# Kernel tuning notes

Measured on AMD Instinct MI355X. Metric: run time of the kernel, lower is better.

The kernel has to match this reference:

```python
import jax, jax.numpy as jnp
import numpy as np

DIM = 384
HEADS = 8


def setup_inputs() -> dict:
    key = jax.random.key(0)
    ks = jax.random.split(key, 8)
    d = DIM
    return {
        "x": jax.random.normal(ks[0], (4, d, 128, 128), jnp.float32),
        "message": jax.random.normal(ks[1], (4, d, 128, 128), jnp.float32),
        "temperature": jnp.ones((HEADS, 1, 1), jnp.float32),
        "qkv_w": jax.random.normal(ks[2], (3 * d, d), jnp.float32) * 0.02,   # 1x1 conv weight
        "dw_w": jax.random.normal(ks[3], (3 * d, 1, 3, 3), jnp.float32) * 0.02,  # depthwise 3x3
        "proj_w": jax.random.normal(ks[4], (d, d), jnp.float32) * 0.02,     # project_out 1x1
        "lin_w": jax.random.normal(ks[5], (d, 2 * d), jnp.float32) * 0.02,  # nn.Linear weight [out,in]
        "lin_b": jnp.zeros((d,), jnp.float32),
    }


def _qkv_branch(t, qkv_w, dw_w):
    # 1x1 conv (pointwise) then depthwise 3x3, groups = 3*dim
    y = jnp.einsum('oc,bchw->bohw', qkv_w, t)
    y = jax.lax.conv_general_dilated(
        y, dw_w, window_strides=(1, 1), padding='SAME',
        dimension_numbers=('NCHW', 'OIHW', 'NCHW'),
        feature_group_count=dw_w.shape[0])
    return jnp.split(y, 3, axis=1)  # q, k, v each [b, dim, h, w]


def _to_heads(t):
    b, c, h, w = t.shape
    return t.reshape(b, HEADS, c // HEADS, h * w)  # [b, head, c, n]


def _l2norm(t):
    # torch F.normalize(dim=-1, eps=1e-12)
    n = jnp.sqrt(jnp.sum(t * t, axis=-1, keepdims=True))
    return t / jnp.maximum(n, 1e-12)


def reference(x, message, temperature, qkv_w, dw_w, proj_w, lin_w, lin_b):
    b, c, h, w = x.shape
    q, k, v = (_to_heads(t) for t in _qkv_branch(x, qkv_w, dw_w))
    q_m, k_m, v_m = (_to_heads(t) for t in _qkv_branch(message, qkv_w, dw_w))

    k_c = jnp.concatenate([k, k_m], axis=2)   # [b, head, 2c, n]
    v_c = jnp.concatenate([v, v_m], axis=2)

    q = _l2norm(q)
    k_c = _l2norm(k_c)
    q_m = _l2norm(q_m)

    # channel attention: [b, head, c, 2c]
    attn1 = jax.nn.softmax(jnp.einsum('bhcn,bhdn->bhcd', q, k_c) * temperature, axis=-1)
    attn2 = jax.nn.softmax(jnp.einsum('bhcn,bhdn->bhcd', q_m, k_c) * temperature, axis=-1)

    out1 = jnp.einsum('bhcd,bhdn->bhcn', attn1, v_c)  # [b, head, c, n]
    out2 = jnp.einsum('bhcd,bhdn->bhcn', attn2, v_c)

    # 'b head c (h w) -> b (h w) (head c)'
    out1 = out1.transpose(0, 3, 1, 2).reshape(b, h * w, c)
    out2 = out2.transpose(0, 3, 1, 2).reshape(b, h * w, c)

    cat = jnp.concatenate([out1, out2], axis=2)  # [b, n, 2c]
    out = cat @ lin_w.T + lin_b                  # [b, n, c]

    # 'b (h w) c -> b c h w'
    out = out.transpose(0, 2, 1).reshape(b, c, h, w)
    out = jnp.einsum('oc,bchw->bohw', proj_w, out)
    return out
```

## Files before the change

kernel.cpp:

```cpp
#include <hip/hip_runtime.h>

typedef unsigned short u16;
typedef unsigned int u32;

#define BATCH 4
#define CDIM 384
#define IMG 128
#define HW 16384
#define QKVC 1152
#define NHEADS 8
#define CHD 48
#define DD2 96
#define KFIN 768

typedef __attribute__((ext_vector_type(8))) short bf16x8;
typedef __attribute__((ext_vector_type(4))) float f32x4;

__device__ __forceinline__ u16 f2bf(float f){
  union { float f; u32 u; } v; v.f = f;
  u32 u = v.u;
  u32 r = (u + 0x7fffu + ((u >> 16) & 1u)) >> 16;
  return (u16)r;
}
__device__ __forceinline__ float bf2f(u16 h){
  union { u32 u; float f; } v; v.u = ((u32)h) << 16;
  return v.f;
}

#define OFF_QKVX  ((size_t)0)
#define OFF_QKVM  ((size_t)150994944)
#define OFF_T     ((size_t)301989888)
#define OFF_SSQ   ((size_t)339738624)
#define OFF_S     ((size_t)339775488)
#define OFF_ATTN  ((size_t)340955136)
#define OFF_AFINB ((size_t)342134784)
#define OFF_W2    ((size_t)344494080)
#define OFF_B2    ((size_t)345673728)
#define OFF_WB    ((size_t)345675264)

typedef __attribute__((address_space(1))) const u32 gas_u32;
typedef __attribute__((address_space(3))) u32 las_u32;
__device__ __forceinline__ void gl_lds16(const u16* g, u16* l){
  __builtin_amdgcn_global_load_lds((gas_u32*)g, (las_u32*)l, 16, 0, 0);
}

__global__ void __launch_bounds__(256) k_w2(const float* __restrict__ proj,
                                            const float* __restrict__ lin,
                                            const float* __restrict__ linb,
                                            const float* __restrict__ qkvw,
                                            float* __restrict__ W2,
                                            float* __restrict__ b2,
                                            u16* __restrict__ Wb){
  int idx = blockIdx.x * 256 + threadIdx.x;
  if (idx < CDIM * KFIN){
    int o = idx / KFIN, d = idx % KFIN;
    float acc = 0.f;
    for (int c = 0; c < CDIM; c++)
      acc = fmaf(proj[o * CDIM + c], lin[c * KFIN + d], acc);
    W2[idx] = acc;
  }
  if (idx < CDIM){
    float acc = 0.f;
    for (int c = 0; c < CDIM; c++)
      acc = fmaf(proj[idx * CDIM + c], linb[c], acc);
    b2[idx] = acc;
  }
  if (idx < QKVC * CDIM) Wb[idx] = f2bf(qkvw[idx]);
}

__global__ void __launch_bounds__(256) k_cvt(const float* __restrict__ x,
                                             const float* __restrict__ msg,
                                             u16* __restrict__ Bt){
  int z = blockIdx.z;
  const float* src = (z < 4 ? x : msg) + (size_t)(z & 3) * CDIM * HW;
  u16* dst = Bt + (size_t)z * HW * CDIM;
  int nb = blockIdx.x * 64, cb = blockIdx.y * 64;
  __shared__ u16 t[64][65];
  int tid = threadIdx.x;
  #pragma unroll
  for (int i = 0; i < 16; i++){
    int idx = tid + i * 256;
    int c = idx >> 6, n = idx & 63;
    t[c][n] = f2bf(src[(size_t)(cb + c) * HW + nb + n]);
  }
  __syncthreads();
  u32* d32 = (u32*)dst;
  #pragma unroll
  for (int i = 0; i < 8; i++){
    int idx = tid + i * 256;
    int n = idx >> 5, cp = idx & 31;
    u32 v = (u32)t[2 * cp][n] | ((u32)t[2 * cp + 1][n] << 16);
    d32[((size_t)(nb + n) * CDIM + cb) / 2 + cp] = v;
  }
}

__global__ void __launch_bounds__(256) k_pw(const u16* __restrict__ A,
                                            const u16* __restrict__ B,
                                            u16* __restrict__ C){
  __shared__ __align__(16) u16 As[2 * 4096];
  __shared__ __align__(16) u16 Bs[2 * 4096];
  int orig = blockIdx.x;
  int swz = (orig & 7) * 144 + (orig >> 3);
  int bx = swz % 9, by = swz / 9;
  int m0 = bx * 128, n0 = by * 128;
  int tid = threadIdx.x;
  int w = tid >> 6, lane = tid & 63;
  int wy = w >> 1, wx = w & 1;
  int lm = lane & 15, q = lane >> 4;

  int srow = w * 16 + (lane >> 2);
  int scol = (lane & 3) * 8;
  const u16* ga = A + (size_t)(m0 + srow) * CDIM + scol;
  const u16* gb = B + (size_t)(n0 + srow) * CDIM + scol;
  u16* la = As + srow * 32 + scol;
  u16* lb = Bs + srow * 32 + scol;

  f32x4 acc[4][4];
  #pragma unroll
  for (int i = 0; i < 4; i++)
    #pragma unroll
    for (int j = 0; j < 4; j++) acc[i][j] = (f32x4){0.f,0.f,0.f,0.f};

#define PW_STAGE(buf, k0) do{ \
    gl_lds16(ga + (k0),             la + (buf) * 4096); \
    gl_lds16(ga + 64*CDIM + (k0),   la + (buf) * 4096 + 2048); \
    gl_lds16(gb + (k0),             lb + (buf) * 4096); \
    gl_lds16(gb + 64*CDIM + (k0),   lb + (buf) * 4096 + 2048); \
  }while(0)

  PW_STAGE(0, 0);
  __syncthreads();
  int cur = 0;
  for (int t = 0; t < 12; t++){
    if (t < 11) PW_STAGE(cur ^ 1, (t + 1) * 32);
    bf16x8 af[4], bfr[4];
    #pragma unroll
    for (int i = 0; i < 4; i++)
      af[i] = *(const bf16x8*)&As[cur * 4096 + (wy * 64 + i * 16 + lm) * 32 + q * 8];
    #pragma unroll
    for (int j = 0; j < 4; j++)
      bfr[j] = *(const bf16x8*)&Bs[cur * 4096 + (wx * 64 + j * 16 + lm) * 32 + q * 8];
    #pragma unroll
    for (int i = 0; i < 4; i++)
      #pragma unroll
      for (int j = 0; j < 4; j++)
        acc[i][j] = __builtin_amdgcn_mfma_f32_16x16x32_bf16(af[i], bfr[j], acc[i][j], 0, 0, 0);
    __syncthreads();
    cur ^= 1;
  }
#undef PW_STAGE
  #pragma unroll
  for (int i = 0; i < 4; i++){
    #pragma unroll
    for (int r = 0; r < 4; r++){
      int row = m0 + wy * 64 + i * 16 + q * 4 + r;
      u16* cp = C + (size_t)row * HW + n0 + wx * 64 + lm;
      #pragma unroll
      for (int j = 0; j < 4; j++)
        cp[j * 16] = f2bf(acc[i][j][r]);
    }
  }
}

__device__ __forceinline__ void loadrow(const u16* __restrict__ src, int r, int cg, float* o){
  if ((unsigned)r >= IMG){
    #pragma unroll
    for (int i = 0; i < 18; i++) o[i] = 0.f;
    return;
  }
  const u16* p = src + (size_t)r * IMG + cg * 16;
  uint4 v0 = *(const uint4*)p;
  uint4 v1 = *(const uint4*)(p + 8);
  u32 ww[8] = {v0.x, v0.y, v0.z, v0.w, v1.x, v1.y, v1.z, v1.w};
  #pragma unroll
  for (int i = 0; i < 8; i++){
    union { u32 u; float f; } lo, hi;
    lo.u = ww[i] << 16;
    hi.u = ww[i] & 0xffff0000u;
    o[1 + 2 * i] = lo.f;
    o[2 + 2 * i] = hi.f;
  }
  o[0]  = (cg > 0) ? bf2f(p[-1]) : 0.f;
  o[17] = (cg < 7) ? bf2f(p[16]) : 0.f;
}

__global__ void __launch_bounds__(256) k_dw2(const u16* __restrict__ T,
                                             const float* __restrict__ dw,
                                             u16* __restrict__ qdst,
                                             u16* __restrict__ vdst,
                                             float* __restrict__ ssq){
  int ch = blockIdx.x;
  const u16* src = T + (size_t)ch * HW;
  u16* dst = (ch < 2 * CDIM) ? qdst + (size_t)ch * HW
                             : vdst + (size_t)(ch - 2 * CDIM) * HW;
  float w[9];
  #pragma unroll
  for (int t = 0; t < 9; t++) w[t] = dw[ch * 9 + t];
  int tid = threadIdx.x;
  int rg = tid >> 3, cg = tid & 7;
  float ss = 0.f;
  #pragma unroll
  for (int rr = 0; rr < 4; rr++){
    int r = rg * 4 + rr;
    float a[18], b[18], c[18];
    loadrow(src, r - 1, cg, a);
    loadrow(src, r,     cg, b);
    loadrow(src, r + 1, cg, c);
    u32 pk[8];
    #pragma unroll
    for (int x = 0; x < 16; x++){
      float acc = w[0] * a[x];
      acc = fmaf(w[1], a[x + 1], acc);
      acc = fmaf(w[2], a[x + 2], acc);
      acc = fmaf(w[3], b[x],     acc);
      acc = fmaf(w[4], b[x + 1], acc);
      acc = fmaf(w[5], b[x + 2], acc);
      acc = fmaf(w[6], c[x],     acc);
      acc = fmaf(w[7], c[x + 1], acc);
      acc = fmaf(w[8], c[x + 2], acc);
      ss = fmaf(acc, acc, ss);
      u16 hv = f2bf(acc);
      if (x & 1) pk[x >> 1] |= (u32)hv << 16;
      else       pk[x >> 1]  = (u32)hv;
    }
    *(uint4*)(dst + (size_t)r * IMG + cg * 16)     = *(uint4*)&pk[0];
    *(uint4*)(dst + (size_t)r * IMG + cg * 16 + 8) = *(uint4*)&pk[4];
  }
  if (ch < 2 * CDIM){
    __shared__ float red[256];
    red[tid] = ss;
    __syncthreads();
    for (int s = 128; s > 0; s >>= 1){
      if (tid < s) red[tid] += red[tid + s];
      __syncthreads();
    }
    if (tid == 0) ssq[ch] = red[0];
  }
}

__global__ void __launch_bounds__(256) k_vt(const u16* __restrict__ Bt,
                                            u16* __restrict__ qkvx,
                                            u16* __restrict__ qkvm){
  int z = blockIdx.z;
  int inp = z >> 2, b = z & 3;
  const u16* vcn = Bt + (size_t)z * HW * CDIM;
  int h = blockIdx.y;
  int n0 = blockIdx.x * 128;
  u16* vt = (h < 4 ? qkvx : qkvm) + ((size_t)b * QKVC + 2 * CDIM) * HW;
  int dbase = (h & 3) * 96 + inp * 48;
  __shared__ u16 tile[48][136];
  int tid = threadIdx.x;
  #pragma unroll
  for (int j = 0; j < 3; j++){
    int i = tid + j * 256;
    int row = i >> 4, c8 = i & 15;
    uint4 v = *(const uint4*)(vcn + (size_t)(h * 48 + row) * HW + n0 + c8 * 8);
    *(uint4*)&tile[row][c8 * 8] = v;
  }
  __syncthreads();
  int n = tid >> 1, half = tid & 1;
  u16* dstp = vt + (size_t)(n0 + n) * CDIM + dbase + half * 24;
  #pragma unroll
  for (int u = 0; u < 3; u++){
    u32 pk[4];
    #pragma unroll
    for (int p = 0; p < 4; p++){
      int c = half * 24 + u * 8 + p * 2;
      pk[p] = (u32)tile[c][n] | ((u32)tile[c + 1][n] << 16);
    }
    *(uint4*)(dstp + u * 8) = *(uint4*)pk;
  }
}

#define LCHUNK 1024
__global__ void __launch_bounds__(256) k_logits_mfma(const u16* __restrict__ qkvx,
                                                     const u16* __restrict__ qkvm,
                                                     float* __restrict__ S){
  int nc = blockIdx.x;
  int bh = blockIdx.y;
  int b = bh & 3, h = bh >> 2;
  int tid = threadIdx.x;
  int w = tid >> 6, lane = tid & 63;
  int wy = w >> 1, wx = w & 1;
  int lm = lane & 15, quad = lane >> 4;

  const u16* ap[3]; const u16* bp[3];
  #pragma unroll
  for (int i = 0; i < 3; i++){
    int g = wy * 48 + i * 16 + lm;
    int c = (g < 48) ? g : g - 48;
    ap[i] = ((g < 48) ? qkvx : qkvm) + ((size_t)b * QKVC + h * CHD + c) * HW;
    int d = wx * 48 + i * 16 + lm;
    int cc = (d < 48) ? d : d - 48;
    bp[i] = ((d < 48) ? qkvx : qkvm) + ((size_t)b * QKVC + CDIM + h * CHD + cc) * HW;
  }
  f32x4 acc[3][3];
  #pragma unroll
  for (int i = 0; i < 3; i++)
    #pragma unroll
    for (int j = 0; j < 3; j++) acc[i][j] = (f32x4){0.f,0.f,0.f,0.f};

  int nbeg = nc * LCHUNK + quad * 8;
  int nend = nc * LCHUNK + LCHUNK;
  for (int n = nbeg; n < nend; n += 32){
    bf16x8 af[3], bfr[3];
    #pragma unroll
    for (int i = 0; i < 3; i++) af[i]  = *(const bf16x8*)(ap[i] + n);
    #pragma unroll
    for (int j = 0; j < 3; j++) bfr[j] = *(const bf16x8*)(bp[j] + n);
    #pragma unroll
    for (int i = 0; i < 3; i++)
      #pragma unroll
      for (int j = 0; j < 3; j++)
        acc[i][j] = __builtin_amdgcn_mfma_f32_16x16x32_bf16(af[i], bfr[j], acc[i][j], 0, 0, 0);
  }
  #pragma unroll
  for (int i = 0; i < 3; i++){
    #pragma unroll
    for (int r = 0; r < 4; r++){
      int g = wy * 48 + i * 16 + quad * 4 + r;
      int iq = (g >= 48) ? 1 : 0;
      int c = iq ? g - 48 : g;
      float* Sp = S + (((size_t)(iq * BATCH + b) * NHEADS + h) * CHD + c) * DD2;
      #pragma unroll
      for (int j = 0; j < 3; j++)
        atomicAdd(&Sp[wx * 48 + j * 16 + lm], acc[i][j][r]);
    }
  }
}

__global__ void __launch_bounds__(128) k_softmax(const float* __restrict__ S,
                                                 const float* __restrict__ ssq,
                                                 const float* __restrict__ temp,
                                                 float* __restrict__ attn){
  int row = blockIdx.x;
  int c = row % CHD;
  int h = (row / CHD) % NHEADS;
  int b = (row / (CHD * NHEADS)) % BATCH;
  int iq = row / (CHD * NHEADS * BATCH);
  int tid = threadIdx.x;
  __shared__ float sh[128];
  const float* Sp = S + (size_t)row * DD2;
  float ssq_q = ssq[(iq * BATCH + b) * QKVC + h * CHD + c];
  float nq = fmaxf(sqrtf(ssq_q), 1e-12f);
  float tmp = temp[h];
  float logit = -1e30f;
  int d = tid;
  if (d < DD2){
    float ssq_k = ssq[((d < CHD ? 0 : 1) * BATCH + b) * QKVC + CDIM + h * CHD + (d % CHD)];
    float nk = fmaxf(sqrtf(ssq_k), 1e-12f);
    logit = Sp[d] * tmp / (nq * nk);
  }
  sh[tid] = logit; __syncthreads();
  for (int s = 64; s > 0; s >>= 1){
    if (tid < s) sh[tid] = fmaxf(sh[tid], sh[tid + s]);
    __syncthreads();
  }
  float mx = sh[0]; __syncthreads();
  float e = (d < DD2) ? expf(logit - mx) : 0.f;
  sh[tid] = e; __syncthreads();
  for (int s = 64; s > 0; s >>= 1){
    if (tid < s) sh[tid] += sh[tid + s];
    __syncthreads();
  }
  float sum = sh[0];
  if (d < DD2) attn[(size_t)row * DD2 + d] = e / sum;
}

__global__ void __launch_bounds__(128) k_mmat(const float* __restrict__ attn,
                                              const float* __restrict__ W2,
                                              u16* __restrict__ AfinB){
  int oz = blockIdx.x;
  int h = blockIdx.y;
  int b = blockIdx.z;
  __shared__ float a1[CHD * DD2];
  __shared__ float a2[CHD * DD2];
  int tid = threadIdx.x;
  const float* A1 = attn + ((size_t)(0 * BATCH + b) * NHEADS + h) * CHD * DD2;
  const float* A2 = attn + ((size_t)(1 * BATCH + b) * NHEADS + h) * CHD * DD2;
  for (int i = tid; i < CHD * DD2; i += 128){ a1[i] = A1[i]; a2[i] = A2[i]; }
  __syncthreads();
  int e = tid;
  if (e < DD2){
    for (int oo = 0; oo < 8; oo++){
      int o = oz * 8 + oo;
      float acc = 0.f;
      #pragma unroll 4
      for (int cc = 0; cc < CHD; cc++){
        acc = fmaf(W2[o * KFIN + h * CHD + cc],        a1[cc * DD2 + e], acc);
        acc = fmaf(W2[o * KFIN + CDIM + h * CHD + cc], a2[cc * DD2 + e], acc);
      }
      AfinB[((size_t)b * CDIM + o) * KFIN + h * DD2 + e] = f2bf(acc);
    }
  }
}

__global__ void __launch_bounds__(256) k_fin(const u16* __restrict__ AfB,
                                             const u16* __restrict__ qkvx,
                                             const u16* __restrict__ qkvm,
                                             const float* __restrict__ b2,
                                             float* __restrict__ out){
  __shared__ __align__(16) u16 As[2 * 4096];
  __shared__ __align__(16) u16 Bs[2 * 4096];
  int orig = blockIdx.x;
  int swz = (orig & 7) * 192 + (orig >> 3);
  int m = swz % 3;
  int rest = swz / 3;
  int n0 = (rest & 127) * 128;
  int bz = rest >> 7;
  int m0 = m * 128;
  int tid = threadIdx.x;
  int w = tid >> 6, lane = tid & 63;
  int wy = w >> 1, wx = w & 1;
  int lm = lane & 15, q = lane >> 4;

  int srow = w * 16 + (lane >> 2);
  int scol = (lane & 3) * 8;
  const u16* A = AfB + (size_t)bz * CDIM * KFIN;
  const u16* ga  = A + (size_t)(m0 + srow) * KFIN + scol;
  const u16* gb0 = qkvx + ((size_t)bz * QKVC + 2 * CDIM) * HW + (size_t)(n0 + srow) * CDIM + scol;
  const u16* gb1 = qkvm + ((size_t)bz * QKVC + 2 * CDIM) * HW + (size_t)(n0 + srow) * CDIM + scol;
  u16* la = As + srow * 32 + scol;
  u16* lb = Bs + srow * 32 + scol;

  f32x4 acc[4][4];
  #pragma unroll
  for (int i = 0; i < 4; i++)
    #pragma unroll
    for (int j = 0; j < 4; j++) acc[i][j] = (f32x4){0.f,0.f,0.f,0.f};

#define FIN_STAGE(buf, t) do{ \
    int hp_ = (t) >= 12; \
    int k0_ = ((t) - hp_ * 12) * 32; \
    const u16* gb_ = hp_ ? gb1 : gb0; \
    gl_lds16(ga + hp_ * CDIM + k0_,            la + (buf) * 4096); \
    gl_lds16(ga + hp_ * CDIM + k0_ + 64*KFIN,  la + (buf) * 4096 + 2048); \
    gl_lds16(gb_ + k0_,                        lb + (buf) * 4096); \
    gl_lds16(gb_ + k0_ + 64*CDIM,              lb + (buf) * 4096 + 2048); \
  }while(0)

  FIN_STAGE(0, 0);
  __syncthreads();
  int cur = 0;
  for (int t = 0; t < 24; t++){
    if (t < 23) FIN_STAGE(cur ^ 1, t + 1);
    bf16x8 af[4], bfr[4];
    #pragma unroll
    for (int i = 0; i < 4; i++)
      af[i] = *(const bf16x8*)&As[cur * 4096 + (wy * 64 + i * 16 + lm) * 32 + q * 8];
    #pragma unroll
    for (int j = 0; j < 4; j++)
      bfr[j] = *(const bf16x8*)&Bs[cur * 4096 + (wx * 64 + j * 16 + lm) * 32 + q * 8];
    #pragma unroll
    for (int i = 0; i < 4; i++)
      #pragma unroll
      for (int j = 0; j < 4; j++)
        acc[i][j] = __builtin_amdgcn_mfma_f32_16x16x32_bf16(af[i], bfr[j], acc[i][j], 0, 0, 0);
    __syncthreads();
    cur ^= 1;
  }
#undef FIN_STAGE
  #pragma unroll
  for (int i = 0; i < 4; i++){
    #pragma unroll
    for (int r = 0; r < 4; r++){
      int row = m0 + wy * 64 + i * 16 + q * 4 + r;
      float bv = b2[row];
      float* cp = out + (size_t)bz * CDIM * HW + (size_t)row * HW + n0 + wx * 64 + lm;
      #pragma unroll
      for (int j = 0; j < 4; j++)
        cp[j * 16] = acc[i][j][r] + bv;
    }
  }
}

extern "C" void kernel_launch(void* const* d_in, const int* in_sizes, int n_in,
                              void* d_out, int out_size, void* d_ws, size_t ws_size,
                              hipStream_t stream){
  const float* x      = (const float*)d_in[0];
  const float* msg    = (const float*)d_in[1];
  const float* temp   = (const float*)d_in[2];
  const float* qkv_w  = (const float*)d_in[3];
  const float* dw_w   = (const float*)d_in[4];
  const float* proj_w = (const float*)d_in[5];
  const float* lin_w  = (const float*)d_in[6];
  const float* lin_b  = (const float*)d_in[7];
  float* out = (float*)d_out;

  char* ws = (char*)d_ws;
  u16*   qkvx  = (u16*)(ws + OFF_QKVX);
  u16*   qkvm  = (u16*)(ws + OFF_QKVM);
  u16*   T     = (u16*)(ws + OFF_T);
  float* ssq   = (float*)(ws + OFF_SSQ);
  float* S     = (float*)(ws + OFF_S);
  float* attn  = (float*)(ws + OFF_ATTN);
  u16*   AfinB = (u16*)(ws + OFF_AFINB);
  float* W2    = (float*)(ws + OFF_W2);
  float* b2    = (float*)(ws + OFF_B2);
  u16*   Wb    = (u16*)(ws + OFF_WB);

  u16* Bt = (u16*)d_out;

  hipMemsetAsync(ws + OFF_S, 0, (OFF_ATTN - OFF_S), stream);

  k_w2<<<dim3((QKVC * CDIM + 255) / 256), dim3(256), 0, stream>>>(
      proj_w, lin_w, lin_b, qkv_w, W2, b2, Wb);

  k_cvt<<<dim3(HW / 64, CDIM / 64, 8), dim3(256), 0, stream>>>(x, msg, Bt);

  for (int z = 0; z < 8; z++){
    int inp = z >> 2, bb = z & 3;
    u16* qdst = (inp ? qkvm : qkvx) + (size_t)bb * QKVC * HW;
    k_pw<<<dim3(QKVC / 128 * (HW / 128)), dim3(256), 0, stream>>>(
        Wb, Bt + (size_t)z * HW * CDIM, T);
    k_dw2<<<dim3(QKVC), dim3(256), 0, stream>>>(
        T, dw_w, qdst, Bt + (size_t)z * HW * CDIM, ssq + (size_t)z * QKVC);
  }

  k_vt<<<dim3(HW / 128, 8, 8), dim3(256), 0, stream>>>(Bt, qkvx, qkvm);

  k_logits_mfma<<<dim3(16, 32), dim3(256), 0, stream>>>(qkvx, qkvm, S);
  k_softmax<<<dim3(2 * BATCH * NHEADS * CHD), dim3(128), 0, stream>>>(S, ssq, temp, attn);
  k_mmat<<<dim3(CDIM / 8, NHEADS, BATCH), dim3(128), 0, stream>>>(attn, W2, AfinB);
  k_fin<<<dim3(3 * (HW / 128) * BATCH), dim3(256), 0, stream>>>(
      AfinB, qkvx, qkvm, b2, out);
}
```

Baseline: 1.017 ms.

## Software-pipeline convert, pointwise GEMM and depthwise conv across fused stage launches

Replaces the per-batch sequence of convert, pointwise GEMM and depthwise kernels with ten launches of one staged kernel. Each launch runs the convert for item t, the GEMM for item t-1 and the depthwise conv for item t-2 concurrently. The GEMM output is double-buffered, with the unused V region of qkvm serving as the second buffer. The V transpose is also fused with the logits kernel into one launch, the depthwise conv reuses rows through a sliding window, and the convert uses float4 loads. The aim is to cut launch count and fill the GPU with independent work, at the cost of more complex block dispatch and higher shared-memory and register pressure in the merged kernel.

```diff
diff --git a/kernel.cpp b/kernel.cpp
--- a/kernel.cpp
+++ b/kernel.cpp
@@ -42,6 +42,13 @@
 typedef __attribute__((address_space(3))) u32 las_u32;
 __device__ __forceinline__ void gl_lds16(const u16* g, u16* l){
   __builtin_amdgcn_global_load_lds((gas_u32*)g, (las_u32*)l, 16, 0, 0);
+}
+
+__device__ __forceinline__ u16* t_row(u16* T0, u16* qkvm, int par, int ch){
+  if (par == 0) return T0 + (size_t)ch * HW;
+  int bq = ch / 384;
+  int rr = ch - bq * 384;
+  return qkvm + ((size_t)bq * QKVC + 2 * CDIM + rr) * HW;
 }
 
 __global__ void __launch_bounds__(256) k_w2(const float* __restrict__ proj,
@@ -68,100 +75,6 @@
   if (idx < QKVC * CDIM) Wb[idx] = f2bf(qkvw[idx]);
 }
 
-__global__ void __launch_bounds__(256) k_cvt(const float* __restrict__ x,
-                                             const float* __restrict__ msg,
-                                             u16* __restrict__ Bt){
-  int z = blockIdx.z;
-  const float* src = (z < 4 ? x : msg) + (size_t)(z & 3) * CDIM * HW;
-  u16* dst = Bt + (size_t)z * HW * CDIM;
-  int nb = blockIdx.x * 64, cb = blockIdx.y * 64;
-  __shared__ u16 t[64][65];
-  int tid = threadIdx.x;
-  #pragma unroll
-  for (int i = 0; i < 16; i++){
-    int idx = tid + i * 256;
-    int c = idx >> 6, n = idx & 63;
-    t[c][n] = f2bf(src[(size_t)(cb + c) * HW + nb + n]);
-  }
-  __syncthreads();
-  u32* d32 = (u32*)dst;
-  #pragma unroll
-  for (int i = 0; i < 8; i++){
-    int idx = tid + i * 256;
-    int n = idx >> 5, cp = idx & 31;
-    u32 v = (u32)t[2 * cp][n] | ((u32)t[2 * cp + 1][n] << 16);
-    d32[((size_t)(nb + n) * CDIM + cb) / 2 + cp] = v;
-  }
-}
-
-__global__ void __launch_bounds__(256) k_pw(const u16* __restrict__ A,
-                                            const u16* __restrict__ B,
-                                            u16* __restrict__ C){
-  __shared__ __align__(16) u16 As[2 * 4096];
-  __shared__ __align__(16) u16 Bs[2 * 4096];
-  int orig = blockIdx.x;
-  int swz = (orig & 7) * 144 + (orig >> 3);
-  int bx = swz % 9, by = swz / 9;
-  int m0 = bx * 128, n0 = by * 128;
-  int tid = threadIdx.x;
-  int w = tid >> 6, lane = tid & 63;
-  int wy = w >> 1, wx = w & 1;
-  int lm = lane & 15, q = lane >> 4;
-
-  int srow = w * 16 + (lane >> 2);
-  int scol = (lane & 3) * 8;
-  const u16* ga = A + (size_t)(m0 + srow) * CDIM + scol;
-  const u16* gb = B + (size_t)(n0 + srow) * CDIM + scol;
-  u16* la = As + srow * 32 + scol;
-  u16* lb = Bs + srow * 32 + scol;
-
-  f32x4 acc[4][4];
-  #pragma unroll
-  for (int i = 0; i < 4; i++)
-    #pragma unroll
-    for (int j = 0; j < 4; j++) acc[i][j] = (f32x4){0.f,0.f,0.f,0.f};
-
-#define PW_STAGE(buf, k0) do{ \
-    gl_lds16(ga + (k0),             la + (buf) * 4096); \
-    gl_lds16(ga + 64*CDIM + (k0),   la + (buf) * 4096 + 2048); \
-    gl_lds16(gb + (k0),             lb + (buf) * 4096); \
-    gl_lds16(gb + 64*CDIM + (k0),   lb + (buf) * 4096 + 2048); \
-  }while(0)
-
-  PW_STAGE(0, 0);
-  __syncthreads();
-  int cur = 0;
-  for (int t = 0; t < 12; t++){
-    if (t < 11) PW_STAGE(cur ^ 1, (t + 1) * 32);
-    bf16x8 af[4], bfr[4];
-    #pragma unroll
-    for (int i = 0; i < 4; i++)
-      af[i] = *(const bf16x8*)&As[cur * 4096 + (wy * 64 + i * 16 + lm) * 32 + q * 8];
-    #pragma unroll
-    for (int j = 0; j < 4; j++)
-      bfr[j] = *(const bf16x8*)&Bs[cur * 4096 + (wx * 64 + j * 16 + lm) * 32 + q * 8];
-    #pragma unroll
-    for (int i = 0; i < 4; i++)
-      #pragma unroll
-      for (int j = 0; j < 4; j++)
-        acc[i][j] = __builtin_amdgcn_mfma_f32_16x16x32_bf16(af[i], bfr[j], acc[i][j], 0, 0, 0);
-    __syncthreads();
-    cur ^= 1;
-  }
-#undef PW_STAGE
-  #pragma unroll
-  for (int i = 0; i < 4; i++){
-    #pragma unroll
-    for (int r = 0; r < 4; r++){
-      int row = m0 + wy * 64 + i * 16 + q * 4 + r;
-      u16* cp = C + (size_t)row * HW + n0 + wx * 64 + lm;
-      #pragma unroll
-      for (int j = 0; j < 4; j++)
-        cp[j * 16] = f2bf(acc[i][j][r]);
-    }
-  }
-}
-
 __device__ __forceinline__ void loadrow(const u16* __restrict__ src, int r, int cg, float* o){
   if ((unsigned)r >= IMG){
     #pragma unroll
@@ -184,147 +97,261 @@
   o[17] = (cg < 7) ? bf2f(p[16]) : 0.f;
 }
 
-__global__ void __launch_bounds__(256) k_dw2(const u16* __restrict__ T,
-                                             const float* __restrict__ dw,
-                                             u16* __restrict__ qdst,
-                                             u16* __restrict__ vdst,
-                                             float* __restrict__ ssq){
-  int ch = blockIdx.x;
-  const u16* src = T + (size_t)ch * HW;
-  u16* dst = (ch < 2 * CDIM) ? qdst + (size_t)ch * HW
-                             : vdst + (size_t)(ch - 2 * CDIM) * HW;
-  float w[9];
-  #pragma unroll
-  for (int t = 0; t < 9; t++) w[t] = dw[ch * 9 + t];
+__global__ void __launch_bounds__(256) k_stage(
+    int t, int npw, int ndw,
+    const u16* __restrict__ Wb, u16* __restrict__ Bt,
+    u16* __restrict__ T0, u16* __restrict__ qkvx, u16* __restrict__ qkvm,
+    const float* __restrict__ x, const float* __restrict__ msg,
+    const float* __restrict__ dww, float* __restrict__ ssq){
+  __shared__ __align__(16) u16 smem[16384];
+  int bid = blockIdx.x;
   int tid = threadIdx.x;
-  int rg = tid >> 3, cg = tid & 7;
-  float ss = 0.f;
-  #pragma unroll
-  for (int rr = 0; rr < 4; rr++){
-    int r = rg * 4 + rr;
-    float a[18], b[18], c[18];
-    loadrow(src, r - 1, cg, a);
-    loadrow(src, r,     cg, b);
-    loadrow(src, r + 1, cg, c);
-    u32 pk[8];
-    #pragma unroll
-    for (int x = 0; x < 16; x++){
-      float acc = w[0] * a[x];
-      acc = fmaf(w[1], a[x + 1], acc);
-      acc = fmaf(w[2], a[x + 2], acc);
-      acc = fmaf(w[3], b[x],     acc);
-      acc = fmaf(w[4], b[x + 1], acc);
-      acc = fmaf(w[5], b[x + 2], acc);
-      acc = fmaf(w[6], c[x],     acc);
-      acc = fmaf(w[7], c[x + 1], acc);
-      acc = fmaf(w[8], c[x + 2], acc);
-      ss = fmaf(acc, acc, ss);
-      u16 hv = f2bf(acc);
-      if (x & 1) pk[x >> 1] |= (u32)hv << 16;
-      else       pk[x >> 1]  = (u32)hv;
-    }
-    *(uint4*)(dst + (size_t)r * IMG + cg * 16)     = *(uint4*)&pk[0];
-    *(uint4*)(dst + (size_t)r * IMG + cg * 16 + 8) = *(uint4*)&pk[4];
-  }
-  if (ch < 2 * CDIM){
-    __shared__ float red[256];
-    red[tid] = ss;
+
+  if (bid < npw){
+    int z = t - 1, par = z & 1;
+    const u16* B = Bt + (size_t)z * HW * CDIM;
+    u16* As = smem;
+    u16* Bs = smem + 8192;
+    int swz = (bid & 7) * 144 + (bid >> 3);
+    int bx = swz % 9, by = swz / 9;
+    int m0 = bx * 128, n0 = by * 128;
+    int w = tid >> 6, lane = tid & 63;
+    int wy = w >> 1, wx = w & 1;
+    int lm = lane & 15, q = lane >> 4;
+
+    int srow = w * 16 + (lane >> 2);
+    int scol = (lane & 3) * 8;
+    const u16* ga = Wb + (size_t)(m0 + srow) * CDIM + scol;
+    const u16* gb = B + (size_t)(n0 + srow) * CDIM + scol;
+    u16* la = As + srow * 32 + scol;
+    u16* lb = Bs + srow * 32 + scol;
+
+    f32x4 acc[4][4];
+    #pragma unroll
+    for (int i = 0; i < 4; i++)
+      #pragma unroll
+      for (int j = 0; j < 4; j++) acc[i][j] = (f32x4){0.f,0.f,0.f,0.f};
+
+#define PW_STAGE(buf, k0) do{ \
+      gl_lds16(ga + (k0),             la + (buf) * 4096); \
+      gl_lds16(ga + 64*CDIM + (k0),   la + (buf) * 4096 + 2048); \
+      gl_lds16(gb + (k0),             lb + (buf) * 4096); \
+      gl_lds16(gb + 64*CDIM + (k0),   lb + (buf) * 4096 + 2048); \
+    }while(0)
+
+    PW_STAGE(0, 0);
     __syncthreads();
-    for (int s = 128; s > 0; s >>= 1){
-      if (tid < s) red[tid] += red[tid + s];
+    int cur = 0;
+    for (int kt = 0; kt < 12; kt++){
+      if (kt < 11) PW_STAGE(cur ^ 1, (kt + 1) * 32);
+      bf16x8 af[4], bfr[4];
+      #pragma unroll
+      for (int i = 0; i < 4; i++)
+        af[i] = *(const bf16x8*)&As[cur * 4096 + (wy * 64 + i * 16 + lm) * 32 + q * 8];
+      #pragma unroll
+      for (int j = 0; j < 4; j++)
+        bfr[j] = *(const bf16x8*)&Bs[cur * 4096 + (wx * 64 + j * 16 + lm) * 32 + q * 8];
+      #pragma unroll
+      for (int i = 0; i < 4; i++)
+        #pragma unroll
+        for (int j = 0; j < 4; j++)
+          acc[i][j] = __builtin_amdgcn_mfma_f32_16x16x32_bf16(af[i], bfr[j], acc[i][j], 0, 0, 0);
       __syncthreads();
-    }
-    if (tid == 0) ssq[ch] = red[0];
-  }
-}
-
-__global__ void __launch_bounds__(256) k_vt(const u16* __restrict__ Bt,
-                                            u16* __restrict__ qkvx,
-                                            u16* __restrict__ qkvm){
-  int z = blockIdx.z;
-  int inp = z >> 2, b = z & 3;
-  const u16* vcn = Bt + (size_t)z * HW * CDIM;
-  int h = blockIdx.y;
-  int n0 = blockIdx.x * 128;
-  u16* vt = (h < 4 ? qkvx : qkvm) + ((size_t)b * QKVC + 2 * CDIM) * HW;
-  int dbase = (h & 3) * 96 + inp * 48;
+      cur ^= 1;
+    }
+#undef PW_STAGE
+    #pragma unroll
+    for (int i = 0; i < 4; i++){
+      #pragma unroll
+      for (int r = 0; r < 4; r++){
+        int row = m0 + wy * 64 + i * 16 + q * 4 + r;
+        u16* cp = t_row(T0, qkvm, par, row) + n0 + wx * 64 + lm;
+        #pragma unroll
+        for (int j = 0; j < 4; j++)
+          cp[j * 16] = f2bf(acc[i][j][r]);
+      }
+    }
+
+  } else if (bid < npw + ndw){
+    int ch = bid - npw;
+    int z = t - 2, par = z & 1;
+    const u16* src = t_row(T0, qkvm, par, ch);
+    u16* dst;
+    if (ch < 2 * CDIM){
+      u16* qd = ((z >> 2) ? qkvm : qkvx) + (size_t)(z & 3) * QKVC * HW;
+      dst = qd + (size_t)ch * HW;
+    } else {
+      dst = Bt + (size_t)z * HW * CDIM + (size_t)(ch - 2 * CDIM) * HW;
+    }
+    float w[9];
+    #pragma unroll
+    for (int t9 = 0; t9 < 9; t9++) w[t9] = dww[ch * 9 + t9];
+    int rg = tid >> 3, cg = tid & 7;
+    int r0 = rg * 4;
+    float ra[18], rb[18], rc[18];
+    loadrow(src, r0 - 1, cg, ra);
+    loadrow(src, r0,     cg, rb);
+    float ss = 0.f;
+    #pragma unroll
+    for (int rr = 0; rr < 4; rr++){
+      int r = r0 + rr;
+      loadrow(src, r + 1, cg, rc);
+      u32 pk[8];
+      #pragma unroll
+      for (int xx = 0; xx < 16; xx++){
+        float a2 = w[0] * ra[xx];
+        a2 = fmaf(w[1], ra[xx + 1], a2);
+        a2 = fmaf(w[2], ra[xx + 2], a2);
+        a2 = fmaf(w[3], rb[xx],     a2);
+        a2 = fmaf(w[4], rb[xx + 1], a2);
+        a2 = fmaf(w[5], rb[xx + 2], a2);
+        a2 = fmaf(w[6], rc[xx],     a2);
+        a2 = fmaf(w[7], rc[xx + 1], a2);
+        a2 = fmaf(w[8], rc[xx + 2], a2);
+        ss = fmaf(a2, a2, ss);
+        u16 hv = f2bf(a2);
+        if (xx & 1) pk[xx >> 1] |= (u32)hv << 16;
+        else        pk[xx >> 1]  = (u32)hv;
+      }
+      *(uint4*)(dst + (size_t)r * IMG + cg * 16)     = *(uint4*)&pk[0];
+      *(uint4*)(dst + (size_t)r * IMG + cg * 16 + 8) = *(uint4*)&pk[4];
+      #pragma unroll
+      for (int ii = 0; ii < 18; ii++){ ra[ii] = rb[ii]; rb[ii] = rc[ii]; }
+    }
+    if (ch < 2 * CDIM){
+      float* red = (float*)smem;
+      red[tid] = ss;
+      __syncthreads();
+      for (int s = 128; s > 0; s >>= 1){
+        if (tid < s) red[tid] += red[tid + s];
+        __syncthreads();
+      }
+      if (tid == 0) ssq[(size_t)z * QKVC + ch] = red[0];
+    }
+
+  } else {
+    int cb = bid - npw - ndw;
+    int z = t;
+    const float* src = (z < 4 ? x : msg) + (size_t)(z & 3) * CDIM * HW;
+    u16* dstz = Bt + (size_t)z * HW * CDIM;
+    int n0 = (cb & 127) * 128;
+    int c0 = (cb >> 7) * 64;
+    u16 (*tile)[130] = (u16(*)[130])smem;
+    #pragma unroll
+    for (int i = 0; i < 8; i++){
+      int c = (tid >> 5) + i * 8;
+      int nq = tid & 31;
+      float4 v = *(const float4*)(src + (size_t)(c0 + c) * HW + n0 + nq * 4);
+      u32 p0 = (u32)f2bf(v.x) | ((u32)f2bf(v.y) << 16);
+      u32 p1 = (u32)f2bf(v.z) | ((u32)f2bf(v.w) << 16);
+      *(u32*)&tile[c][nq * 4]     = p0;
+      *(u32*)&tile[c][nq * 4 + 2] = p1;
+    }
+    __syncthreads();
+    #pragma unroll
+    for (int u = 0; u < 2; u++){
+      int idx = tid + u * 256;
+      int n = idx >> 2, j = idx & 3;
+      u32 pk[8];
+      #pragma unroll
+      for (int p = 0; p < 8; p++)
+        pk[p] = (u32)tile[j * 16 + 2 * p][n] | ((u32)tile[j * 16 + 2 * p + 1][n] << 16);
+      u16* dp = dstz + (size_t)(n0 + n) * CDIM + c0 + j * 16;
+      *(uint4*)dp       = *(uint4*)&pk[0];
+      *(uint4*)(dp + 8) = *(uint4*)&pk[4];
+    }
+  }
+}
+
+#define LCHUNK 1024
+__global__ void __launch_bounds__(256) k_tail(u16* __restrict__ qkvx,
+                                              u16* __restrict__ qkvm,
+                                              float* __restrict__ S,
+                                              const u16* __restrict__ Bt){
   __shared__ u16 tile[48][136];
+  int bid = blockIdx.x;
   int tid = threadIdx.x;
-  #pragma unroll
-  for (int j = 0; j < 3; j++){
-    int i = tid + j * 256;
-    int row = i >> 4, c8 = i & 15;
-    uint4 v = *(const uint4*)(vcn + (size_t)(h * 48 + row) * HW + n0 + c8 * 8);
-    *(uint4*)&tile[row][c8 * 8] = v;
-  }
-  __syncthreads();
-  int n = tid >> 1, half = tid & 1;
-  u16* dstp = vt + (size_t)(n0 + n) * CDIM + dbase + half * 24;
-  #pragma unroll
-  for (int u = 0; u < 3; u++){
-    u32 pk[4];
-    #pragma unroll
-    for (int p = 0; p < 4; p++){
-      int c = half * 24 + u * 8 + p * 2;
-      pk[p] = (u32)tile[c][n] | ((u32)tile[c + 1][n] << 16);
-    }
-    *(uint4*)(dstp + u * 8) = *(uint4*)pk;
-  }
-}
-
-#define LCHUNK 1024
-__global__ void __launch_bounds__(256) k_logits_mfma(const u16* __restrict__ qkvx,
-                                                     const u16* __restrict__ qkvm,
-                                                     float* __restrict__ S){
-  int nc = blockIdx.x;
-  int bh = blockIdx.y;
-  int b = bh & 3, h = bh >> 2;
-  int tid = threadIdx.x;
-  int w = tid >> 6, lane = tid & 63;
-  int wy = w >> 1, wx = w & 1;
-  int lm = lane & 15, quad = lane >> 4;
-
-  const u16* ap[3]; const u16* bp[3];
-  #pragma unroll
-  for (int i = 0; i < 3; i++){
-    int g = wy * 48 + i * 16 + lm;
-    int c = (g < 48) ? g : g - 48;
-    ap[i] = ((g < 48) ? qkvx : qkvm) + ((size_t)b * QKVC + h * CHD + c) * HW;
-    int d = wx * 48 + i * 16 + lm;
-    int cc = (d < 48) ? d : d - 48;
-    bp[i] = ((d < 48) ? qkvx : qkvm) + ((size_t)b * QKVC + CDIM + h * CHD + cc) * HW;
-  }
-  f32x4 acc[3][3];
-  #pragma unroll
-  for (int i = 0; i < 3; i++)
-    #pragma unroll
-    for (int j = 0; j < 3; j++) acc[i][j] = (f32x4){0.f,0.f,0.f,0.f};
-
-  int nbeg = nc * LCHUNK + quad * 8;
-  int nend = nc * LCHUNK + LCHUNK;
-  for (int n = nbeg; n < nend; n += 32){
-    bf16x8 af[3], bfr[3];
-    #pragma unroll
-    for (int i = 0; i < 3; i++) af[i]  = *(const bf16x8*)(ap[i] + n);
-    #pragma unroll
-    for (int j = 0; j < 3; j++) bfr[j] = *(const bf16x8*)(bp[j] + n);
+
+  if (bid < 512){
+    int nc = bid & 15;
+    int bh = bid >> 4;
+    int b = bh & 3, h = bh >> 2;
+    int w = tid >> 6, lane = tid & 63;
+    int wy = w >> 1, wx = w & 1;
+    int lm = lane & 15, quad = lane >> 4;
+
+    const u16* ap[3]; const u16* bp[3];
+    #pragma unroll
+    for (int i = 0; i < 3; i++){
+      int g = wy * 48 + i * 16 + lm;
+      int c = (g < 48) ? g : g - 48;
+      ap[i] = ((g < 48) ? qkvx : qkvm) + ((size_t)b * QKVC + h * CHD + c) * HW;
+      int d = wx * 48 + i * 16 + lm;
+      int cc = (d < 48) ? d : d - 48;
+      bp[i] = ((d < 48) ? qkvx : qkvm) + ((size_t)b * QKVC + CDIM + h * CHD + cc) * HW;
+    }
+    f32x4 acc[3][3];
     #pragma unroll
     for (int i = 0; i < 3; i++)
       #pragma unroll
-      for (int j = 0; j < 3; j++)
-        acc[i][j] = __builtin_amdgcn_mfma_f32_16x16x32_bf16(af[i], bfr[j], acc[i][j], 0, 0, 0);
-  }
-  #pragma unroll
-  for (int i = 0; i < 3; i++){
-    #pragma unroll
-    for (int r = 0; r < 4; r++){
-      int g = wy * 48 + i * 16 + quad * 4 + r;
-      int iq = (g >= 48) ? 1 : 0;
-      int c = iq ? g - 48 : g;
-      float* Sp = S + (((size_t)(iq * BATCH + b) * NHEADS + h) * CHD + c) * DD2;
-      #pragma unroll
-      for (int j = 0; j < 3; j++)
-        atomicAdd(&Sp[wx * 48 + j * 16 + lm], acc[i][j][r]);
+      for (int j = 0; j < 3; j++) acc[i][j] = (f32x4){0.f,0.f,0.f,0.f};
+
+    int nbeg = nc * LCHUNK + quad * 8;
+    int nend = nc * LCHUNK + LCHUNK;
+    for (int n = nbeg; n < nend; n += 32){
+      bf16x8 af[3], bfr[3];
+      #pragma unroll
+      for (int i = 0; i < 3; i++) af[i]  = *(const bf16x8*)(ap[i] + n);
+      #pragma unroll
+      for (int j = 0; j < 3; j++) bfr[j] = *(const bf16x8*)(bp[j] + n);
+      #pragma unroll
+      for (int i = 0; i < 3; i++)
+        #pragma unroll
+        for (int j = 0; j < 3; j++)
+          acc[i][j] = __builtin_amdgcn_mfma_f32_16x16x32_bf16(af[i], bfr[j], acc[i][j], 0, 0, 0);
+    }
+    #pragma unroll
+    for (int i = 0; i < 3; i++){
+      #pragma unroll
+      for (int r = 0; r < 4; r++){
+        int g = wy * 48 + i * 16 + quad * 4 + r;
+        int iq = (g >= 48) ? 1 : 0;
+        int c = iq ? g - 48 : g;
+        float* Sp = S + (((size_t)(iq * BATCH + b) * NHEADS + h) * CHD + c) * DD2;
+        #pragma unroll
+        for (int j = 0; j < 3; j++)
+          atomicAdd(&Sp[wx * 48 + j * 16 + lm], acc[i][j][r]);
+      }
+    }
+  } else {
+    int v = bid - 512;
+    int nb = v & 127;
+    int h = (v >> 7) & 7;
+    int z = v >> 10;
+    int inp = z >> 2, b = z & 3;
+    const u16* vcn = Bt + (size_t)z * HW * CDIM;
+    int n0 = nb * 128;
+    u16* vt = (h < 4 ? qkvx : qkvm) + ((size_t)b * QKVC + 2 * CDIM) * HW;
+    int dbase = (h & 3) * 96 + inp * 48;
+    #pragma unroll
+    for (int j = 0; j < 3; j++){
+      int i = tid + j * 256;
+      int row = i >> 4, c8 = i & 15;
+      uint4 vv = *(const uint4*)(vcn + (size_t)(h * 48 + row) * HW + n0 + c8 * 8);
+      *(uint4*)&tile[row][c8 * 8] = vv;
+    }
+    __syncthreads();
+    int n = tid >> 1, half = tid & 1;
+    u16* dstp = vt + (size_t)(n0 + n) * CDIM + dbase + half * 24;
+    #pragma unroll
+    for (int u = 0; u < 3; u++){
+      u32 pk[4];
+      #pragma unroll
+      for (int p = 0; p < 4; p++){
+        int c = half * 24 + u * 8 + p * 2;
+        pk[p] = (u32)tile[c][n] | ((u32)tile[c + 1][n] << 16);
+      }
+      *(uint4*)(dstp + u * 8) = *(uint4*)pk;
     }
   }
 }
@@ -490,7 +517,7 @@
   char* ws = (char*)d_ws;
   u16*   qkvx  = (u16*)(ws + OFF_QKVX);
   u16*   qkvm  = (u16*)(ws + OFF_QKVM);
-  u16*   T     = (u16*)(ws + OFF_T);
+  u16*   T0    = (u16*)(ws + OFF_T);
   float* ssq   = (float*)(ws + OFF_SSQ);
   float* S     = (float*)(ws + OFF_S);
   float* attn  = (float*)(ws + OFF_ATTN);
@@ -506,20 +533,15 @@
   k_w2<<<dim3((QKVC * CDIM + 255) / 256), dim3(256), 0, stream>>>(
       proj_w, lin_w, lin_b, qkv_w, W2, b2, Wb);
 
-  k_cvt<<<dim3(HW / 64, CDIM / 64, 8), dim3(256), 0, stream>>>(x, msg, Bt);
-
-  for (int z = 0; z < 8; z++){
-    int inp = z >> 2, bb = z & 3;
-    u16* qdst = (inp ? qkvm : qkvx) + (size_t)bb * QKVC * HW;
-    k_pw<<<dim3(QKVC / 128 * (HW / 128)), dim3(256), 0, stream>>>(
-        Wb, Bt + (size_t)z * HW * CDIM, T);
-    k_dw2<<<dim3(QKVC), dim3(256), 0, stream>>>(
-        T, dw_w, qdst, Bt + (size_t)z * HW * CDIM, ssq + (size_t)z * QKVC);
-  }
-
-  k_vt<<<dim3(HW / 128, 8, 8), dim3(256), 0, stream>>>(Bt, qkvx, qkvm);
-
-  k_logits_mfma<<<dim3(16, 32), dim3(256), 0, stream>>>(qkvx, qkvm, S);
+  for (int t = 0; t < 10; t++){
+    int npw  = (t >= 1 && t <= 8) ? 1152 : 0;
+    int ndw  = (t >= 2) ? 1152 : 0;
+    int ncvt = (t < 8) ? 768 : 0;
+    k_stage<<<dim3(npw + ndw + ncvt), dim3(256), 0, stream>>>(
+        t, npw, ndw, Wb, Bt, T0, qkvx, qkvm, x, msg, dw_w, ssq);
+  }
+
+  k_tail<<<dim3(512 + 8192), dim3(256), 0, stream>>>(qkvx, qkvm, S, Bt);
   k_softmax<<<dim3(2 * BATCH * NHEADS * CHD), dim3(128), 0, stream>>>(S, ssq, temp, attn);
   k_mmat<<<dim3(CDIM / 8, NHEADS, BATCH), dim3(128), 0, stream>>>(attn, W2, AfinB);
   k_fin<<<dim3(3 * (HW / 128) * BATCH), dim3(256), 0, stream>>>(
```

Result: faster. 843.3 us (-17.1%).
